# Kernel tuning notes

Hardware: AMD Instinct MI355X
Metric: run time of the kernel (lower is better)

Reference implementation:

```python
import jax, jax.numpy as jnp
import numpy as np


def _excl_cumsum(f, axis, reverse):
    """Exclusive (strict) cumulative sum along `axis`, optionally from the far end."""
    if reverse:
        c = jnp.flip(jnp.cumsum(jnp.flip(f, axis), axis=axis), axis)
    else:
        c = jnp.cumsum(f, axis=axis)
    return c - f  # inclusive minus self = exclusive (strict inequality)


def _dir_sum(f, direction):
    """Strict directional 2D prefix sum over [B,T,H,W].
    NE: sum over h' < h (north) and w' > w (east).
    SW: sum over h' > h and w' < w.
    SE: sum over h' > h and w' > w.
    """
    rev_h, rev_w = {"NE": (False, True), "SW": (True, False), "SE": (True, True)}[direction]
    return _excl_cumsum(_excl_cumsum(f, 2, rev_h), 3, rev_w)


def _weight(alpha, x):
    # per-tree, per-channel linear weighting contracted over channels: [T,C],[B,C,H,W] -> [B,T,H,W]
    return jnp.einsum("tc,bchw->bthw", alpha, x)


def setup_inputs() -> dict:
    key = jax.random.key(0)
    ks = jax.random.split(key, 7)
    B, C, H, W = 16, 32, 256, 256
    T2 = 8  # num_trees // 2
    return {
        "x": jax.random.normal(ks[0], (B, C, H, W), dtype=jnp.float32),
        "alpha_1": jax.random.normal(ks[1], (T2, C), dtype=jnp.float32),
        "alpha_2": jax.random.normal(ks[2], (T2, C), dtype=jnp.float32),
        "alpha_3": jax.random.normal(ks[3], (T2, C), dtype=jnp.float32),
        "alpha_1p": jax.random.normal(ks[4], (T2, C), dtype=jnp.float32),
        "alpha_2p": jax.random.normal(ks[5], (T2, C), dtype=jnp.float32),
        "alpha_3p": jax.random.normal(ks[6], (T2, C), dtype=jnp.float32),
    }


def reference(x, alpha_1, alpha_2, alpha_3, alpha_1p, alpha_2p, alpha_3p):
    # Linear tree: root(alpha_1) --NE--> node(alpha_2) --SW--> leaf(alpha_3)
    v3 = _weight(alpha_3, x)
    v2 = _weight(alpha_2, x) * _dir_sum(v3, "SW")
    linear = _weight(alpha_1, x) * _dir_sum(v2, "NE")
    # Cherry tree: root(alpha_1p) with children SW->leaf(alpha_3p), SE->leaf(alpha_2p)
    cherry = (
        _weight(alpha_1p, x)
        * _dir_sum(_weight(alpha_3p, x), "SW")
        * _dir_sum(_weight(alpha_2p, x), "SE")
    )
    # cat=True: concatenate the two tree families along the tree/channel axis
    return jnp.concatenate([linear, cherry], axis=1)  # [B, num_trees, H, W]
```

## Files before the change

kernel.cpp:

```cpp
#include <hip/hip_runtime.h>

#define B   16
#define C   32
#define T2  8
#define H   256
#define W   256
#define NF  (B * T2 * H * W)


__device__ __forceinline__ float wave_incl_scan(float s, int lane) {
#pragma unroll
  for (int d = 1; d < 64; d <<= 1) {
    float n = __shfl_up(s, (unsigned)d, 64);
    if (lane >= d) s += n;
  }
  return s;
}

__global__ __launch_bounds__(256) void k_weight6(
    const float* __restrict__ x,
    const float* __restrict__ a1,  const float* __restrict__ a2,
    const float* __restrict__ a3,  const float* __restrict__ a1p,
    const float* __restrict__ a2p, const float* __restrict__ a3p,
    float* __restrict__ ws, float* __restrict__ out) {
  int pix = blockIdx.x * 256 + threadIdx.x;
  int b  = pix >> 16;
  int hw = pix & 65535;
  const float* xb = x + (size_t)(b * C) * 65536 + hw;

  float acc1[T2] = {}, acc2[T2] = {}, acc3[T2] = {};
  float acc1p[T2] = {}, acc2p[T2] = {}, acc3p[T2] = {};

#pragma unroll
  for (int c = 0; c < C; ++c) {
    float xv = xb[(size_t)c * 65536];
#pragma unroll
    for (int t = 0; t < T2; ++t) {
      acc3[t]  = fmaf(a3 [t * C + c], xv, acc3[t]);
      acc2[t]  = fmaf(a2 [t * C + c], xv, acc2[t]);
      acc1[t]  = fmaf(a1 [t * C + c], xv, acc1[t]);
      acc3p[t] = fmaf(a3p[t * C + c], xv, acc3p[t]);
      acc2p[t] = fmaf(a2p[t * C + c], xv, acc2p[t]);
      acc1p[t] = fmaf(a1p[t * C + c], xv, acc1p[t]);
    }
  }

#pragma unroll
  for (int t = 0; t < T2; ++t) {
    size_t so = ((size_t)(b * T2 + t) << 16) + hw;
    ws[so]               = acc3[t];
    ws[(size_t)NF + so]  = acc2[t];
    ws[2ull * NF + so]   = acc3p[t];
    ws[3ull * NF + so]   = acc2p[t];
    out[((size_t)(b * 16 + t)     << 16) + hw] = acc1[t];
    out[((size_t)(b * 16 + 8 + t) << 16) + hw] = acc1p[t];
  }
}

__global__ __launch_bounds__(256) void k_weight3(
    const float* __restrict__ x,
    const float* __restrict__ aA, const float* __restrict__ aB,
    const float* __restrict__ aC,
    float* __restrict__ ws0, float* __restrict__ ws1,
    float* __restrict__ out, int outoff) {
  int pix = blockIdx.x * 256 + threadIdx.x;
  int b  = pix >> 16;
  int hw = pix & 65535;
  const float* xb = x + (size_t)(b * C) * 65536 + hw;

  float accA[T2] = {}, accB[T2] = {}, accC[T2] = {};

#pragma unroll
  for (int c = 0; c < C; ++c) {
    float xv = xb[(size_t)c * 65536];
#pragma unroll
    for (int t = 0; t < T2; ++t) {
      accA[t] = fmaf(aA[t * C + c], xv, accA[t]);
      accB[t] = fmaf(aB[t * C + c], xv, accB[t]);
      accC[t] = fmaf(aC[t * C + c], xv, accC[t]);
    }
  }

#pragma unroll
  for (int t = 0; t < T2; ++t) {
    size_t so = ((size_t)(b * T2 + t) << 16) + hw;
    ws0[so] = accB[t];
    ws1[so] = accC[t];
    out[((size_t)(b * 16 + outoff + t) << 16) + hw] = accA[t];
  }
}

__global__ __launch_bounds__(256) void k_colscan_rev(float* __restrict__ base_) {
  float* base = base_ + ((size_t)blockIdx.x << 16) + threadIdx.x;
  float run = 0.f;
#pragma unroll 8
  for (int h = 255; h >= 0; --h) {
    float v = base[h << 8];
    base[h << 8] = run;
    run += v;
  }
}

__global__ __launch_bounds__(256) void k_colscan_fwd(float* __restrict__ base_) {
  float* base = base_ + ((size_t)blockIdx.x << 16) + threadIdx.x;
  float run = 0.f;
#pragma unroll 8
  for (int h = 0; h < 256; ++h) {
    float v = base[h << 8];
    base[h << 8] = run;
    run += v;
  }
}

__global__ __launch_bounds__(256) void k_row_v2(float* __restrict__ wsA,
                                                const float* __restrict__ wsB) {
  int lane = threadIdx.x & 63;
  int r = blockIdx.x * 4 + (threadIdx.x >> 6);
  float4* arow = (float4*)(wsA + (size_t)r * 256);
  const float4* brow = (const float4*)(wsB + (size_t)r * 256);

  float4 a = arow[lane];
  float s = a.x + a.y + a.z + a.w;
  float incl = wave_incl_scan(s, lane);
  float excl = incl - s;
  float e0 = excl, e1 = e0 + a.x, e2 = e1 + a.y, e3 = e2 + a.z;

  float4 bq = brow[lane];
  float4 o;
  o.x = bq.x * e0; o.y = bq.y * e1; o.z = bq.z * e2; o.w = bq.w * e3;
  arow[lane] = o;
}

__global__ __launch_bounds__(256) void k_final_linear(const float* __restrict__ wsV,
                                                      float* __restrict__ out) {
  int lane = threadIdx.x & 63;
  int r = blockIdx.x * 4 + (threadIdx.x >> 6);
  const float4* vrow = (const float4*)(wsV + (size_t)r * 256);
  float4 a = vrow[lane];
  float s = a.x + a.y + a.z + a.w;
  float incl = wave_incl_scan(s, lane);
  float excl = incl - s;
  float total = __shfl(incl, 63, 64);
  float r0 = total - excl - a.x;
  float r1 = r0 - a.y;
  float r2 = r1 - a.z;
  float r3 = r2 - a.w;

  int b = r >> 11, t = (r >> 8) & 7, h = r & 255;
  float* orow = out + ((size_t)((b * 16 + t) * 256 + h)) * 256;
  float4 f = ((const float4*)orow)[lane];
  float4 o;
  o.x = f.x * r0; o.y = f.y * r1; o.z = f.z * r2; o.w = f.w * r3;
  ((float4*)orow)[lane] = o;
}

__global__ __launch_bounds__(256) void k_cherry(const float* __restrict__ wsAp,
                                                const float* __restrict__ wsBp,
                                                float* __restrict__ out) {
  int lane = threadIdx.x & 63;
  int r = blockIdx.x * 4 + (threadIdx.x >> 6);
  const float4* ap = (const float4*)(wsAp + (size_t)r * 256);
  const float4* bp = (const float4*)(wsBp + (size_t)r * 256);
  float4 a  = ap[lane];
  float4 bq = bp[lane];
  float sa = a.x + a.y + a.z + a.w;
  float sb = bq.x + bq.y + bq.z + bq.w;
  float ia = wave_incl_scan(sa, lane);
  float ib = wave_incl_scan(sb, lane);
  float ea = ia - sa;
  float eb = ib - sb;
  float tb = __shfl(ib, 63, 64);

  float fa0 = ea, fa1 = fa0 + a.x, fa2 = fa1 + a.y, fa3 = fa2 + a.z;
  float rb0 = tb - eb - bq.x;
  float rb1 = rb0 - bq.y;
  float rb2 = rb1 - bq.z;
  float rb3 = rb2 - bq.w;

  int b = r >> 11, t = (r >> 8) & 7, h = r & 255;
  float* orow = out + ((size_t)((b * 16 + 8 + t) * 256 + h)) * 256;
  float4 f = ((const float4*)orow)[lane];
  float4 o;
  o.x = f.x * fa0 * rb0;
  o.y = f.y * fa1 * rb1;
  o.z = f.z * fa2 * rb2;
  o.w = f.w * fa3 * rb3;
  ((float4*)orow)[lane] = o;
}

extern "C" void kernel_launch(void* const* d_in, const int* in_sizes, int n_in,
                              void* d_out, int out_size, void* d_ws, size_t ws_size,
                              hipStream_t stream) {
  const float* x   = (const float*)d_in[0];
  const float* a1  = (const float*)d_in[1];
  const float* a2  = (const float*)d_in[2];
  const float* a3  = (const float*)d_in[3];
  const float* a1p = (const float*)d_in[4];
  const float* a2p = (const float*)d_in[5];
  const float* a3p = (const float*)d_in[6];
  float* out = (float*)d_out;
  float* ws  = (float*)d_ws;

  const size_t field_bytes = (size_t)NF * 4;

  if (ws_size >= 4 * field_bytes) {
    k_weight6<<<4096, 256, 0, stream>>>(x, a1, a2, a3, a1p, a2p, a3p, ws, out);
    k_colscan_rev<<<128, 256, 0, stream>>>(ws);
    k_colscan_rev<<<256, 256, 0, stream>>>(ws + 2ull * NF);
    k_row_v2<<<8192, 256, 0, stream>>>(ws, ws + NF);
    k_colscan_fwd<<<128, 256, 0, stream>>>(ws);
    k_final_linear<<<8192, 256, 0, stream>>>(ws, out);
    k_cherry<<<8192, 256, 0, stream>>>(ws + 2ull * NF, ws + 3ull * NF, out);
  } else {
    float* ws0 = ws;
    float* ws1 = ws + NF;
    k_weight3<<<4096, 256, 0, stream>>>(x, a1, a3, a2, ws0, ws1, out, 0);
    k_colscan_rev<<<128, 256, 0, stream>>>(ws0);
    k_row_v2<<<8192, 256, 0, stream>>>(ws0, ws1);
    k_colscan_fwd<<<128, 256, 0, stream>>>(ws0);
    k_final_linear<<<8192, 256, 0, stream>>>(ws0, out);
    k_weight3<<<4096, 256, 0, stream>>>(x, a1p, a3p, a2p, ws0, ws1, out, 8);
    k_colscan_rev<<<256, 256, 0, stream>>>(ws0);
    k_cherry<<<8192, 256, 0, stream>>>(ws0, ws1, out);
  }
}
```

Measured before the change: 393.7 us.

## Chunk column scans and fuse them with row scans via block-local tiles

Adds a new path that splits each 256-row column scan into 8 chunks of 32 rows. A small chunk-sum kernel computes per-chunk column totals, and each block then combines the preceding chunk offsets with its own column scan in shared memory. Each block then runs the row scan and the multiply in the same kernel. This replaces the low-parallelism column-scan kernels (128-256 blocks) and removes several full-field read/write passes, at the cost of an extra small workspace region and a chunk-sum pass. The path is only taken when the workspace is large enough.

```diff
diff --git a/kernel.cpp b/kernel.cpp
--- a/kernel.cpp
+++ b/kernel.cpp
@@ -6,6 +6,9 @@
 #define H   256
 #define W   256
 #define NF  (B * T2 * H * W)
+#define NCH 8
+#define CH  32
+#define SUMSZ (B * T2 * NCH * W)
 
 
 __device__ __forceinline__ float wave_incl_scan(float s, int lane) {
@@ -57,6 +60,171 @@
   }
 }
 
+__global__ __launch_bounds__(256) void k_chunksums(float* __restrict__ ws) {
+  int f    = blockIdx.x >> 10;
+  int bid  = blockIdx.x & 1023;
+  int slice = bid >> 3, chunk = bid & 7;
+  int w = threadIdx.x;
+  const size_t fieldOff[3] = {0, 2ull * NF, 3ull * NF};
+  const float* base = ws + fieldOff[f] + ((size_t)slice << 16) + (size_t)(chunk * CH) * W + w;
+  float s = 0.f;
+#pragma unroll
+  for (int h = 0; h < CH; ++h) s += base[h * W];
+  float* sums = ws + 4ull * NF + (size_t)f * SUMSZ;
+  sums[(size_t)(slice * NCH + chunk) * W + w] = s;
+}
+
+__global__ __launch_bounds__(256) void k_linear_mid(float* __restrict__ ws) {
+  __shared__ float tile[CH][W];
+  __shared__ float colpart[4][W];
+  int slice = blockIdx.x >> 3, chunk = blockIdx.x & 7;
+  int tid = threadIdx.x, lane = tid & 63, wv = tid >> 6;
+
+  const float* S3 = ws + 4ull * NF;
+  float* Sv2      = ws + 4ull * NF + 3ull * SUMSZ;
+  float* fbase  = ws + ((size_t)slice << 16) + (size_t)(chunk * CH) * W;
+  const float* f2base = ws + (size_t)NF + ((size_t)slice << 16) + (size_t)(chunk * CH) * W;
+
+  {
+    int w = tid;
+    float run = 0.f;
+#pragma unroll
+    for (int c = 0; c < NCH; ++c)
+      if (c > chunk) run += S3[(size_t)(slice * NCH + c) * W + w];
+#pragma unroll
+    for (int h = CH - 1; h >= 0; --h) {
+      float v = fbase[(size_t)h * W + w];
+      tile[h][w] = run;
+      run += v;
+    }
+  }
+  __syncthreads();
+
+  float4 cs = {0.f, 0.f, 0.f, 0.f};
+#pragma unroll
+  for (int i = 0; i < 8; ++i) {
+    int h = wv * 8 + i;
+    float4 a = *(const float4*)&tile[h][lane * 4];
+    float s = a.x + a.y + a.z + a.w;
+    float incl = wave_incl_scan(s, lane);
+    float excl = incl - s;
+    float e0 = excl, e1 = e0 + a.x, e2 = e1 + a.y, e3 = e2 + a.z;
+    float4 f = *(const float4*)&f2base[(size_t)h * W + lane * 4];
+    float4 o;
+    o.x = f.x * e0; o.y = f.y * e1; o.z = f.z * e2; o.w = f.w * e3;
+    *(float4*)&fbase[(size_t)h * W + lane * 4] = o;
+    cs.x += o.x; cs.y += o.y; cs.z += o.z; cs.w += o.w;
+  }
+  *(float4*)&colpart[wv][lane * 4] = cs;
+  __syncthreads();
+  {
+    int w = tid;
+    float sv = colpart[0][w] + colpart[1][w] + colpart[2][w] + colpart[3][w];
+    Sv2[(size_t)(slice * NCH + chunk) * W + w] = sv;
+  }
+}
+
+__global__ __launch_bounds__(256) void k_linear_fin(const float* __restrict__ ws,
+                                                    float* __restrict__ out) {
+  __shared__ float tile[CH][W];
+  int slice = blockIdx.x >> 3, chunk = blockIdx.x & 7;
+  int tid = threadIdx.x, lane = tid & 63, wv = tid >> 6;
+
+  const float* Sv2 = ws + 4ull * NF + 3ull * SUMSZ;
+  const float* vbase = ws + ((size_t)slice << 16) + (size_t)(chunk * CH) * W;
+
+  {
+    int w = tid;
+    float run = 0.f;
+#pragma unroll
+    for (int c = 0; c < NCH; ++c)
+      if (c < chunk) run += Sv2[(size_t)(slice * NCH + c) * W + w];
+#pragma unroll
+    for (int h = 0; h < CH; ++h) {
+      float v = vbase[(size_t)h * W + w];
+      tile[h][w] = run;
+      run += v;
+    }
+  }
+  __syncthreads();
+
+  int b = slice >> 3, t = slice & 7;
+  float* obase = out + ((size_t)(b * 16 + t) << 16) + (size_t)(chunk * CH) * W;
+#pragma unroll
+  for (int i = 0; i < 8; ++i) {
+    int h = wv * 8 + i;
+    float4 a = *(const float4*)&tile[h][lane * 4];
+    float s = a.x + a.y + a.z + a.w;
+    float incl = wave_incl_scan(s, lane);
+    float excl = incl - s;
+    float total = __shfl(incl, 63, 64);
+    float r0 = total - excl - a.x;
+    float r1 = r0 - a.y, r2 = r1 - a.z, r3 = r2 - a.w;
+    float4 f = *(const float4*)&obase[(size_t)h * W + lane * 4];
+    float4 o;
+    o.x = f.x * r0; o.y = f.y * r1; o.z = f.z * r2; o.w = f.w * r3;
+    *(float4*)&obase[(size_t)h * W + lane * 4] = o;
+  }
+}
+
+__global__ __launch_bounds__(256) void k_cherry2(const float* __restrict__ ws,
+                                                 float* __restrict__ out) {
+  __shared__ float tA[CH][W];
+  __shared__ float tB[CH][W];
+  int slice = blockIdx.x >> 3, chunk = blockIdx.x & 7;
+  int tid = threadIdx.x, lane = tid & 63, wv = tid >> 6;
+
+  const float* S3p = ws + 4ull * NF + 1ull * SUMSZ;
+  const float* S2p = ws + 4ull * NF + 2ull * SUMSZ;
+  const float* abase = ws + 2ull * NF + ((size_t)slice << 16) + (size_t)(chunk * CH) * W;
+  const float* bbase = ws + 3ull * NF + ((size_t)slice << 16) + (size_t)(chunk * CH) * W;
+
+  {
+    int w = tid;
+    float runA = 0.f, runB = 0.f;
+#pragma unroll
+    for (int c = 0; c < NCH; ++c)
+      if (c > chunk) {
+        runA += S3p[(size_t)(slice * NCH + c) * W + w];
+        runB += S2p[(size_t)(slice * NCH + c) * W + w];
+      }
+#pragma unroll
+    for (int h = CH - 1; h >= 0; --h) {
+      float va = abase[(size_t)h * W + w];
+      float vb = bbase[(size_t)h * W + w];
+      tA[h][w] = runA; runA += va;
+      tB[h][w] = runB; runB += vb;
+    }
+  }
+  __syncthreads();
+
+  int b = slice >> 3, t = slice & 7;
+  float* obase = out + ((size_t)(b * 16 + 8 + t) << 16) + (size_t)(chunk * CH) * W;
+#pragma unroll
+  for (int i = 0; i < 8; ++i) {
+    int h = wv * 8 + i;
+    float4 a = *(const float4*)&tA[h][lane * 4];
+    float4 bq = *(const float4*)&tB[h][lane * 4];
+    float sa = a.x + a.y + a.z + a.w;
+    float sb = bq.x + bq.y + bq.z + bq.w;
+    float ia = wave_incl_scan(sa, lane);
+    float ib = wave_incl_scan(sb, lane);
+    float ea = ia - sa;
+    float eb = ib - sb;
+    float tb = __shfl(ib, 63, 64);
+    float fa0 = ea, fa1 = fa0 + a.x, fa2 = fa1 + a.y, fa3 = fa2 + a.z;
+    float rb0 = tb - eb - bq.x;
+    float rb1 = rb0 - bq.y, rb2 = rb1 - bq.z, rb3 = rb2 - bq.w;
+    float4 f = *(const float4*)&obase[(size_t)h * W + lane * 4];
+    float4 o;
+    o.x = f.x * fa0 * rb0;
+    o.y = f.y * fa1 * rb1;
+    o.z = f.z * fa2 * rb2;
+    o.w = f.w * fa3 * rb3;
+    *(float4*)&obase[(size_t)h * W + lane * 4] = o;
+  }
+}
+
 __global__ __launch_bounds__(256) void k_weight3(
     const float* __restrict__ x,
     const float* __restrict__ aA, const float* __restrict__ aB,
@@ -67,9 +235,7 @@
   int b  = pix >> 16;
   int hw = pix & 65535;
   const float* xb = x + (size_t)(b * C) * 65536 + hw;
-
   float accA[T2] = {}, accB[T2] = {}, accC[T2] = {};
-
 #pragma unroll
   for (int c = 0; c < C; ++c) {
     float xv = xb[(size_t)c * 65536];
@@ -80,7 +246,6 @@
       accC[t] = fmaf(aC[t * C + c], xv, accC[t]);
     }
   }
-
 #pragma unroll
   for (int t = 0; t < T2; ++t) {
     size_t so = ((size_t)(b * T2 + t) << 16) + hw;
@@ -118,13 +283,11 @@
   int r = blockIdx.x * 4 + (threadIdx.x >> 6);
   float4* arow = (float4*)(wsA + (size_t)r * 256);
   const float4* brow = (const float4*)(wsB + (size_t)r * 256);
-
   float4 a = arow[lane];
   float s = a.x + a.y + a.z + a.w;
   float incl = wave_incl_scan(s, lane);
   float excl = incl - s;
   float e0 = excl, e1 = e0 + a.x, e2 = e1 + a.y, e3 = e2 + a.z;
-
   float4 bq = brow[lane];
   float4 o;
   o.x = bq.x * e0; o.y = bq.y * e1; o.z = bq.z * e2; o.w = bq.w * e3;
@@ -142,10 +305,7 @@
   float excl = incl - s;
   float total = __shfl(incl, 63, 64);
   float r0 = total - excl - a.x;
-  float r1 = r0 - a.y;
-  float r2 = r1 - a.z;
-  float r3 = r2 - a.w;
-
+  float r1 = r0 - a.y, r2 = r1 - a.z, r3 = r2 - a.w;
   int b = r >> 11, t = (r >> 8) & 7, h = r & 255;
   float* orow = out + ((size_t)((b * 16 + t) * 256 + h)) * 256;
   float4 f = ((const float4*)orow)[lane];
@@ -170,13 +330,9 @@
   float ea = ia - sa;
   float eb = ib - sb;
   float tb = __shfl(ib, 63, 64);
-
   float fa0 = ea, fa1 = fa0 + a.x, fa2 = fa1 + a.y, fa3 = fa2 + a.z;
   float rb0 = tb - eb - bq.x;
-  float rb1 = rb0 - bq.y;
-  float rb2 = rb1 - bq.z;
-  float rb3 = rb2 - bq.w;
-
+  float rb1 = rb0 - bq.y, rb2 = rb1 - bq.z, rb3 = rb2 - bq.w;
   int b = r >> 11, t = (r >> 8) & 7, h = r & 255;
   float* orow = out + ((size_t)((b * 16 + 8 + t) * 256 + h)) * 256;
   float4 f = ((const float4*)orow)[lane];
@@ -202,8 +358,15 @@
   float* ws  = (float*)d_ws;
 
   const size_t field_bytes = (size_t)NF * 4;
-
-  if (ws_size >= 4 * field_bytes) {
+  const size_t need_fast2  = 4 * field_bytes + 4ull * SUMSZ * 4;
+
+  if (ws_size >= need_fast2) {
+    k_weight6<<<4096, 256, 0, stream>>>(x, a1, a2, a3, a1p, a2p, a3p, ws, out);
+    k_chunksums<<<3072, 256, 0, stream>>>(ws);
+    k_linear_mid<<<1024, 256, 0, stream>>>(ws);
+    k_linear_fin<<<1024, 256, 0, stream>>>(ws, out);
+    k_cherry2<<<1024, 256, 0, stream>>>(ws, out);
+  } else if (ws_size >= 4 * field_bytes) {
     k_weight6<<<4096, 256, 0, stream>>>(x, a1, a2, a3, a1p, a2p, a3p, ws, out);
     k_colscan_rev<<<128, 256, 0, stream>>>(ws);
     k_colscan_rev<<<256, 256, 0, stream>>>(ws + 2ull * NF);
```

Result: faster. 338.7 us (-14.0%).
